# Kernel tuning notes

Measured on AMD Instinct MI355X. Metric: run time of the kernel, lower is better.

The kernel has to match this reference:

```python
import jax, jax.numpy as jnp
import numpy as np

HEAD_DIM = 64
EMBED_DIM = 1024

def setup_inputs() -> dict:
    key = jax.random.key(0)
    k1, k2, k3, k4 = jax.random.split(key, 4)
    x = jax.random.normal(k1, (4, 4096, EMBED_DIM), dtype=jnp.float32)
    # nn.Linear(embed_dim, head_dim, bias=False): weight shape (head_dim, embed_dim)
    s = 1.0 / np.sqrt(EMBED_DIM)
    Wq = jax.random.uniform(k2, (HEAD_DIM, EMBED_DIM), jnp.float32, -s, s)
    Wk = jax.random.uniform(k3, (HEAD_DIM, EMBED_DIM), jnp.float32, -s, s)
    Wv = jax.random.uniform(k4, (HEAD_DIM, EMBED_DIM), jnp.float32, -s, s)
    return {"x": x, "Wq": Wq, "Wk": Wk, "Wv": Wv}

def reference(x, Wq, Wk, Wv):
    # Faithful to source: V = self.key(x), i.e. uses Wk (Wv is an unused param).
    n_ctx = x.shape[1]
    Q = jnp.einsum('bse,de->bsd', x, Wq)
    K = jnp.einsum('bse,de->bsd', x, Wk)
    V = jnp.einsum('bse,de->bsd', x, Wk)
    scale = 1.0 / jnp.sqrt(jnp.asarray(K.shape[-1], x.dtype))
    scores = jnp.einsum('bqd,bkd->bqk', Q, K) * scale  # [b, n_ctx, n_ctx]
    causal = jnp.tril(jnp.ones((n_ctx, n_ctx), dtype=bool))
    scores = jnp.where(causal, scores, jnp.asarray(-jnp.inf, scores.dtype))
    attn = jax.nn.softmax(scores, axis=-1)
    # dropout(p=0.2) omitted: reference runs in eval mode (identity)
    out = jnp.einsum('bqk,bkd->bqd', attn, V)
    return out
```

## Files before the change

kernel.cpp:

```cpp
#include <hip/hip_runtime.h>

typedef _Float16 f16;
typedef _Float16 f16x8 __attribute__((ext_vector_type(8)));
typedef _Float16 f16x4 __attribute__((ext_vector_type(4)));
typedef float f32x4 __attribute__((ext_vector_type(4)));

#define S_LEN 4096
#define B_SZ  4
#define E_DIM 1024
#define D_DIM 64
#define NROWS (B_SZ * S_LEN)
#define QSCALE (0.125f * 1.44269504088896f)
#define SMAX 8.0f

__device__ __forceinline__ float exp2g(float x) { return __builtin_amdgcn_exp2f(x); }

__global__ __launch_bounds__(256) void wpack_kernel(const float* __restrict__ Wq,
                                                    const float* __restrict__ Wk,
                                                    f16* __restrict__ Bp) {
    int id = blockIdx.x * 256 + threadIdx.x;
    int lane = id & 63, kc = (id >> 6) & 31, n = id >> 11;
    int row = n * 16 + (lane & 15);
    int col = kc * 32 + (lane >> 4) * 8;
    const float* src = (row < 64) ? (Wq + (long)row * E_DIM + col)
                                  : (Wk + (long)(row - 64) * E_DIM + col);
    float4 v0 = ((const float4*)src)[0];
    float4 v1 = ((const float4*)src)[1];
    f16x8 h = {(f16)v0.x, (f16)v0.y, (f16)v0.z, (f16)v0.w,
               (f16)v1.x, (f16)v1.y, (f16)v1.z, (f16)v1.w};
    *(f16x8*)(Bp + (long)id * 8) = h;
}

__global__ __launch_bounds__(512, 2) void proj_kernel(const float* __restrict__ x,
                                                      const f16* __restrict__ Bp,
                                                      f16* __restrict__ Qh,
                                                      f16* __restrict__ Khp,
                                                      f16* __restrict__ Kvp) {
    __shared__ union {
        float xs[2][64][68];
        float ro[8][16][68];
    } sm;

    const int tid  = threadIdx.x;
    const int wav  = tid >> 6;
    const int w_m  = wav >> 1;
    const int w_n  = wav & 1;
    const int lane = tid & 63;
    const int l15  = lane & 15;
    const int quad = lane >> 4;
    const long m0  = (long)blockIdx.x * 64;

    f32x4 acc[4];
#pragma unroll
    for (int n = 0; n < 4; n++) acc[n] = (f32x4){0.f, 0.f, 0.f, 0.f};

    float4 ra[2];
    const int r0[2]  = { (tid * 2 + 0) >> 4,  (tid * 2 + 1) >> 4 };
    (void)r0;

#pragma unroll
    for (int j = 0; j < 2; j++) {
        int idx = j * 512 + tid;
        int row = idx >> 4, c4 = idx & 15;
        ra[j] = *(const float4*)(x + (m0 + row) * E_DIM + c4 * 4);
    }
#pragma unroll
    for (int j = 0; j < 2; j++) {
        int idx = j * 512 + tid;
        int row = idx >> 4, c4 = idx & 15;
        *(f32x4*)&sm.xs[0][row][c4 * 4] = (f32x4){ra[j].x, ra[j].y, ra[j].z, ra[j].w};
    }
    __syncthreads();

    for (int c = 0; c < 16; c++) {
        const int cur = c & 1;
        if (c + 1 < 16) {
#pragma unroll
            for (int j = 0; j < 2; j++) {
                int idx = j * 512 + tid;
                int row = idx >> 4, c4 = idx & 15;
                ra[j] = *(const float4*)(x + (m0 + row) * E_DIM + (c + 1) * 64 + c4 * 4);
            }
        }
#pragma unroll
        for (int kf = 0; kf < 2; kf++) {
            f32x4 a0 = *(const f32x4*)&sm.xs[cur][w_m * 16 + l15][kf * 32 + quad * 8];
            f32x4 a1 = *(const f32x4*)&sm.xs[cur][w_m * 16 + l15][kf * 32 + quad * 8 + 4];
            f16x8 A = {(f16)a0[0], (f16)a0[1], (f16)a0[2], (f16)a0[3],
                       (f16)a1[0], (f16)a1[1], (f16)a1[2], (f16)a1[3]};
            const int kc = c * 2 + kf;
#pragma unroll
            for (int nn = 0; nn < 4; nn++) {
                const int n = w_n * 4 + nn;
                f16x8 B = *(const f16x8*)(Bp + (((long)n * 32 + kc) * 64 + lane) * 8);
                acc[nn] = __builtin_amdgcn_mfma_f32_16x16x32_f16(A, B, acc[nn], 0, 0, 0);
            }
        }
        if (c + 1 < 16) {
#pragma unroll
            for (int j = 0; j < 2; j++) {
                int idx = j * 512 + tid;
                int row = idx >> 4, c4 = idx & 15;
                *(f32x4*)&sm.xs[cur ^ 1][row][c4 * 4] = (f32x4){ra[j].x, ra[j].y, ra[j].z, ra[j].w};
            }
        }
        __syncthreads();
    }

    const int s = wav;
#pragma unroll
    for (int nn = 0; nn < 4; nn++)
#pragma unroll
        for (int r = 0; r < 4; r++)
            sm.ro[s][quad * 4 + r][nn * 16 + l15] = acc[nn][r];
    __syncthreads();

    if (w_n == 0) {
        float q[16];
#pragma unroll
        for (int g = 0; g < 4; g++)
            *(f32x4*)&q[g * 4] = *(const f32x4*)&sm.ro[s][l15][quad * 16 + g * 4];
        f16 o[16];
#pragma unroll
        for (int i = 0; i < 16; i++) o[i] = (f16)(q[i] * QSCALE);
        f16* dst = Qh + (m0 + w_m * 16 + l15) * 64 + quad * 16;
        *(f16x8*)dst       = *(f16x8*)&o[0];
        *(f16x8*)(dst + 8) = *(f16x8*)&o[8];
    } else {
        const long chunk = blockIdx.x;
#pragma unroll
        for (int kf = 0; kf < 2; kf++) {
            f32x4 k0 = *(const f32x4*)&sm.ro[s][l15][kf * 32 + quad * 8];
            f32x4 k1 = *(const f32x4*)&sm.ro[s][l15][kf * 32 + quad * 8 + 4];
            f16x8 h = {(f16)k0[0], (f16)k0[1], (f16)k0[2], (f16)k0[3],
                       (f16)k1[0], (f16)k1[1], (f16)k1[2], (f16)k1[3]};
            *(f16x8*)(Khp + chunk * 4096 + (w_m * 2 + kf) * 512 + lane * 8) = h;
        }
        f16 t16[16];
#pragma unroll
        for (int nn = 0; nn < 4; nn++)
#pragma unroll
            for (int j = 0; j < 4; j++)
                t16[nn * 4 + j] = (f16)sm.ro[s][quad * 4 + j][nn * 16 + l15];
        f16* dst = Kvp + chunk * 4096 + w_m * 1024 + lane * 16;
        *(f16x8*)dst       = *(f16x8*)&t16[0];
        *(f16x8*)(dst + 8) = *(f16x8*)&t16[8];
    }
}

__global__ __launch_bounds__(256, 2) void attn_kernel(const f16* __restrict__ Qh,
                                                      const f16* __restrict__ Khp,
                                                      const f16* __restrict__ Kvp,
                                                      float* __restrict__ Out) {
    __shared__ float Ro[4][32][68];
    __shared__ float Rl[4][32];

    const int tid  = threadIdx.x;
    const int w    = tid >> 6;
    const int lane = tid & 63;
    const int l15  = lane & 15;
    const int quad = lane >> 4;

    const int bid = blockIdx.x;
    int q32, b;
    if (bid < 256) { q32 = 127 - (bid >> 2); b = bid & 3; }
    else           { int k = bid - 256; q32 = k >> 2; b = k & 3; }
    const int q0   = q32 * 32;
    const int jmax = q32 >> 1;

    const f16* Qb = Qh + (long)b * S_LEN * 64;
    f16x8 Aq[2][2];
#pragma unroll
    for (int g = 0; g < 2; g++)
#pragma unroll
        for (int kf = 0; kf < 2; kf++)
            Aq[g][kf] = *(const f16x8*)(Qb + (long)(q0 + g * 16 + l15) * 64 + kf * 32 + quad * 8);

    const f16x4 ones = {(f16)1.f, (f16)1.f, (f16)1.f, (f16)1.f};
    f32x4 O[2][4];
    f32x4 Lacc[2];
#pragma unroll
    for (int g = 0; g < 2; g++) {
        Lacc[g] = (f32x4){0.f, 0.f, 0.f, 0.f};
#pragma unroll
        for (int n = 0; n < 4; n++) O[g][n] = (f32x4){0.f, 0.f, 0.f, 0.f};
    }

    const long cb = (long)b * 64;

#define LOADKA(buf, jj)                                                        \
    {                                                                          \
        const f16* p_ = Khp + (cb + (jj)) * 4096 + lane * 8;                   \
        _Pragma("unroll")                                                      \
        for (int q8 = 0; q8 < 8; q8++) buf[q8] = *(const f16x8*)(p_ + q8 * 512);\
    }

#define COMPUTE(buf, jj)                                                       \
    {                                                                          \
        const f16* kv_ = Kvp + (cb + (jj)) * 4096 + lane * 16;                 \
        const int tlim = ((jj) == jmax) ? (((q0 + 31 - jmax * 64) >> 4) + 1) : 4; \
        _Pragma("unroll")                                                      \
        for (int t = 0; t < 4; t++) {                                          \
            if (t < tlim) {                                                    \
                f32x4 St0 = (f32x4){0.f, 0.f, 0.f, 0.f};                       \
                f32x4 St1 = (f32x4){0.f, 0.f, 0.f, 0.f};                       \
                St0 = __builtin_amdgcn_mfma_f32_16x16x32_f16(buf[t * 2],     Aq[0][0], St0, 0, 0, 0); \
                St0 = __builtin_amdgcn_mfma_f32_16x16x32_f16(buf[t * 2 + 1], Aq[0][1], St0, 0, 0, 0); \
                St1 = __builtin_amdgcn_mfma_f32_16x16x32_f16(buf[t * 2],     Aq[1][0], St1, 0, 0, 0); \
                St1 = __builtin_amdgcn_mfma_f32_16x16x32_f16(buf[t * 2 + 1], Aq[1][1], St1, 0, 0, 0); \
                if ((jj) == jmax) {                                            \
                    int kc_ = jmax * 64 + t * 16 + quad * 4;                   \
                    _Pragma("unroll")                                          \
                    for (int r = 0; r < 4; r++) {                              \
                        if (kc_ + r > q0 + l15)      St0[r] = -1e30f;          \
                        if (kc_ + r > q0 + 16 + l15) St1[r] = -1e30f;          \
                    }                                                          \
                }                                                              \
                f16x4 P0, P1;                                                  \
                _Pragma("unroll")                                              \
                for (int r = 0; r < 4; r++) {                                  \
                    P0[r] = (f16)exp2g(St0[r] - SMAX);                         \
                    P1[r] = (f16)exp2g(St1[r] - SMAX);                         \
                }                                                              \
                Lacc[0] = __builtin_amdgcn_mfma_f32_16x16x16f16(P0, ones, Lacc[0], 0, 0, 0); \
                Lacc[1] = __builtin_amdgcn_mfma_f32_16x16x16f16(P1, ones, Lacc[1], 0, 0, 0); \
                f16x8 v0 = *(const f16x8*)(kv_ + t * 1024);                    \
                f16x8 v1 = *(const f16x8*)(kv_ + t * 1024 + 8);                \
                f16x4 b0 = __builtin_shufflevector(v0, v0, 0, 1, 2, 3);        \
                f16x4 b1 = __builtin_shufflevector(v0, v0, 4, 5, 6, 7);        \
                f16x4 b2 = __builtin_shufflevector(v1, v1, 0, 1, 2, 3);        \
                f16x4 b3 = __builtin_shufflevector(v1, v1, 4, 5, 6, 7);        \
                O[0][0] = __builtin_amdgcn_mfma_f32_16x16x16f16(P0, b0, O[0][0], 0, 0, 0); \
                O[0][1] = __builtin_amdgcn_mfma_f32_16x16x16f16(P0, b1, O[0][1], 0, 0, 0); \
                O[0][2] = __builtin_amdgcn_mfma_f32_16x16x16f16(P0, b2, O[0][2], 0, 0, 0); \
                O[0][3] = __builtin_amdgcn_mfma_f32_16x16x16f16(P0, b3, O[0][3], 0, 0, 0); \
                O[1][0] = __builtin_amdgcn_mfma_f32_16x16x16f16(P1, b0, O[1][0], 0, 0, 0); \
                O[1][1] = __builtin_amdgcn_mfma_f32_16x16x16f16(P1, b1, O[1][1], 0, 0, 0); \
                O[1][2] = __builtin_amdgcn_mfma_f32_16x16x16f16(P1, b2, O[1][2], 0, 0, 0); \
                O[1][3] = __builtin_amdgcn_mfma_f32_16x16x16f16(P1, b3, O[1][3], 0, 0, 0); \
            }                                                                  \
        }                                                                      \
    }

    f16x8 kaA[8], kaB[8];
    int j = w;
    if (j <= jmax) LOADKA(kaA, j);
    while (j <= jmax) {
        if (j + 4 <= jmax) LOADKA(kaB, j + 4);
        COMPUTE(kaA, j);
        j += 4;
        if (j > jmax) break;
        if (j + 4 <= jmax) LOADKA(kaA, j + 4);
        COMPUTE(kaB, j);
        j += 4;
    }
#undef LOADKA
#undef COMPUTE

#pragma unroll
    for (int g = 0; g < 2; g++) {
#pragma unroll
        for (int n = 0; n < 4; n++)
#pragma unroll
            for (int r = 0; r < 4; r++)
                Ro[w][g * 16 + quad * 4 + r][n * 16 + l15] = O[g][n][r];
        if (l15 == 0)
#pragma unroll
            for (int r = 0; r < 4; r++)
                Rl[w][g * 16 + quad * 4 + r] = Lacc[g][r];
    }
    __syncthreads();

    const int row = tid >> 3;
    const int c0  = (tid & 7) * 8;
    float sum[8];
#pragma unroll
    for (int i = 0; i < 8; i++) sum[i] = 0.f;
    float lt = 0.f;
#pragma unroll
    for (int w4 = 0; w4 < 4; w4++) {
        lt += Rl[w4][row];
#pragma unroll
        for (int g4 = 0; g4 < 2; g4++) {
            f32x4 u = *(const f32x4*)&Ro[w4][row][c0 + g4 * 4];
#pragma unroll
            for (int i = 0; i < 4; i++) sum[g4 * 4 + i] += u[i];
        }
    }
    float inv = 1.0f / lt;
    float* dst = Out + ((long)b * S_LEN + q0 + row) * 64 + c0;
    *(float4*)dst       = make_float4(sum[0] * inv, sum[1] * inv, sum[2] * inv, sum[3] * inv);
    *(float4*)(dst + 4) = make_float4(sum[4] * inv, sum[5] * inv, sum[6] * inv, sum[7] * inv);
}

extern "C" void kernel_launch(void* const* d_in, const int* in_sizes, int n_in,
                              void* d_out, int out_size, void* d_ws, size_t ws_size,
                              hipStream_t stream) {
    const float* x  = (const float*)d_in[0];
    const float* Wq = (const float*)d_in[1];
    const float* Wk = (const float*)d_in[2];
    float* out = (float*)d_out;

    f16* Qh  = (f16*)d_ws;
    f16* Bp  = Qh + (long)NROWS * D_DIM;
    f16* Khp = Bp + (long)128 * E_DIM;
    f16* Kvp = Khp + (long)NROWS * D_DIM;

    wpack_kernel<<<dim3(64), dim3(256), 0, stream>>>(Wq, Wk, Bp);
    proj_kernel<<<dim3(NROWS / 64), dim3(512), 0, stream>>>(x, Bp, Qh, Khp, Kvp);
    attn_kernel<<<dim3(B_SZ * 128), dim3(256), 0, stream>>>(Qh, Khp, Kvp, out);
}
```

Baseline: 155.6 us.

## Prefetch V tiles with K in attention; halve projection block size

```diff
diff --git a/kernel.cpp b/kernel.cpp
--- a/kernel.cpp
+++ b/kernel.cpp
@@ -31,42 +31,39 @@
     *(f16x8*)(Bp + (long)id * 8) = h;
 }
 
-__global__ __launch_bounds__(512, 2) void proj_kernel(const float* __restrict__ x,
-                                                      const f16* __restrict__ Bp,
-                                                      f16* __restrict__ Qh,
-                                                      f16* __restrict__ Khp,
-                                                      f16* __restrict__ Kvp) {
+__global__ __launch_bounds__(256) void proj_kernel(const float* __restrict__ x,
+                                                   const f16* __restrict__ Bp,
+                                                   f16* __restrict__ Qh,
+                                                   f16* __restrict__ Khp,
+                                                   f16* __restrict__ Kvp) {
     __shared__ union {
-        float xs[2][64][68];
-        float ro[8][16][68];
+        float xs[2][32][68];
+        float ro[4][16][68];
     } sm;
 
     const int tid  = threadIdx.x;
-    const int wav  = tid >> 6;
-    const int w_m  = wav >> 1;
-    const int w_n  = wav & 1;
+    const int w    = tid >> 6;
+    const int w_m  = w >> 1;
+    const int w_n  = w & 1;
     const int lane = tid & 63;
     const int l15  = lane & 15;
     const int quad = lane >> 4;
-    const long m0  = (long)blockIdx.x * 64;
+    const long m0  = (long)blockIdx.x * 32;
 
     f32x4 acc[4];
 #pragma unroll
     for (int n = 0; n < 4; n++) acc[n] = (f32x4){0.f, 0.f, 0.f, 0.f};
 
     float4 ra[2];
-    const int r0[2]  = { (tid * 2 + 0) >> 4,  (tid * 2 + 1) >> 4 };
-    (void)r0;
-
 #pragma unroll
     for (int j = 0; j < 2; j++) {
-        int idx = j * 512 + tid;
+        int idx = j * 256 + tid;
         int row = idx >> 4, c4 = idx & 15;
         ra[j] = *(const float4*)(x + (m0 + row) * E_DIM + c4 * 4);
     }
 #pragma unroll
     for (int j = 0; j < 2; j++) {
-        int idx = j * 512 + tid;
+        int idx = j * 256 + tid;
         int row = idx >> 4, c4 = idx & 15;
         *(f32x4*)&sm.xs[0][row][c4 * 4] = (f32x4){ra[j].x, ra[j].y, ra[j].z, ra[j].w};
     }
@@ -77,7 +74,7 @@
         if (c + 1 < 16) {
 #pragma unroll
             for (int j = 0; j < 2; j++) {
-                int idx = j * 512 + tid;
+                int idx = j * 256 + tid;
                 int row = idx >> 4, c4 = idx & 15;
                 ra[j] = *(const float4*)(x + (m0 + row) * E_DIM + (c + 1) * 64 + c4 * 4);
             }
@@ -99,7 +96,7 @@
         if (c + 1 < 16) {
 #pragma unroll
             for (int j = 0; j < 2; j++) {
-                int idx = j * 512 + tid;
+                int idx = j * 256 + tid;
                 int row = idx >> 4, c4 = idx & 15;
                 *(f32x4*)&sm.xs[cur ^ 1][row][c4 * 4] = (f32x4){ra[j].x, ra[j].y, ra[j].z, ra[j].w};
             }
@@ -107,19 +104,18 @@
         __syncthreads();
     }
 
-    const int s = wav;
 #pragma unroll
     for (int nn = 0; nn < 4; nn++)
 #pragma unroll
         for (int r = 0; r < 4; r++)
-            sm.ro[s][quad * 4 + r][nn * 16 + l15] = acc[nn][r];
+            sm.ro[w][quad * 4 + r][nn * 16 + l15] = acc[nn][r];
     __syncthreads();
 
     if (w_n == 0) {
         float q[16];
 #pragma unroll
         for (int g = 0; g < 4; g++)
-            *(f32x4*)&q[g * 4] = *(const f32x4*)&sm.ro[s][l15][quad * 16 + g * 4];
+            *(f32x4*)&q[g * 4] = *(const f32x4*)&sm.ro[w][l15][quad * 16 + g * 4];
         f16 o[16];
 #pragma unroll
         for (int i = 0; i < 16; i++) o[i] = (f16)(q[i] * QSCALE);
@@ -127,31 +123,32 @@
         *(f16x8*)dst       = *(f16x8*)&o[0];
         *(f16x8*)(dst + 8) = *(f16x8*)&o[8];
     } else {
-        const long chunk = blockIdx.x;
+        const long chunk = blockIdx.x >> 1;
+        const int  t     = (blockIdx.x & 1) * 2 + w_m;
 #pragma unroll
         for (int kf = 0; kf < 2; kf++) {
-            f32x4 k0 = *(const f32x4*)&sm.ro[s][l15][kf * 32 + quad * 8];
-            f32x4 k1 = *(const f32x4*)&sm.ro[s][l15][kf * 32 + quad * 8 + 4];
+            f32x4 k0 = *(const f32x4*)&sm.ro[w][l15][kf * 32 + quad * 8];
+            f32x4 k1 = *(const f32x4*)&sm.ro[w][l15][kf * 32 + quad * 8 + 4];
             f16x8 h = {(f16)k0[0], (f16)k0[1], (f16)k0[2], (f16)k0[3],
                        (f16)k1[0], (f16)k1[1], (f16)k1[2], (f16)k1[3]};
-            *(f16x8*)(Khp + chunk * 4096 + (w_m * 2 + kf) * 512 + lane * 8) = h;
+            *(f16x8*)(Khp + chunk * 4096 + (t * 2 + kf) * 512 + lane * 8) = h;
         }
         f16 t16[16];
 #pragma unroll
         for (int nn = 0; nn < 4; nn++)
 #pragma unroll
             for (int j = 0; j < 4; j++)
-                t16[nn * 4 + j] = (f16)sm.ro[s][quad * 4 + j][nn * 16 + l15];
-        f16* dst = Kvp + chunk * 4096 + w_m * 1024 + lane * 16;
+                t16[nn * 4 + j] = (f16)sm.ro[w][quad * 4 + j][nn * 16 + l15];
+        f16* dst = Kvp + chunk * 4096 + t * 1024 + lane * 16;
         *(f16x8*)dst       = *(f16x8*)&t16[0];
         *(f16x8*)(dst + 8) = *(f16x8*)&t16[8];
     }
 }
 
-__global__ __launch_bounds__(256, 2) void attn_kernel(const f16* __restrict__ Qh,
-                                                      const f16* __restrict__ Khp,
-                                                      const f16* __restrict__ Kvp,
-                                                      float* __restrict__ Out) {
+__global__ __launch_bounds__(256) void attn_kernel(const f16* __restrict__ Qh,
+                                                   const f16* __restrict__ Khp,
+                                                   const f16* __restrict__ Kvp,
+                                                   float* __restrict__ Out) {
     __shared__ float Ro[4][32][68];
     __shared__ float Rl[4][32];
 
@@ -188,26 +185,31 @@
 
     const long cb = (long)b * 64;
 
-#define LOADKA(buf, jj)                                                        \
+#define LOADK(bufa, bufv, jj)                                                  \
     {                                                                          \
-        const f16* p_ = Khp + (cb + (jj)) * 4096 + lane * 8;                   \
+        const f16* pa_ = Khp + (cb + (jj)) * 4096 + lane * 8;                  \
         _Pragma("unroll")                                                      \
-        for (int q8 = 0; q8 < 8; q8++) buf[q8] = *(const f16x8*)(p_ + q8 * 512);\
-    }
-
-#define COMPUTE(buf, jj)                                                       \
+        for (int q8 = 0; q8 < 8; q8++) bufa[q8] = *(const f16x8*)(pa_ + q8 * 512); \
+        const f16* pv_ = Kvp + (cb + (jj)) * 4096 + lane * 16;                 \
+        _Pragma("unroll")                                                      \
+        for (int t = 0; t < 4; t++) {                                          \
+            bufv[t * 2]     = *(const f16x8*)(pv_ + t * 1024);                 \
+            bufv[t * 2 + 1] = *(const f16x8*)(pv_ + t * 1024 + 8);             \
+        }                                                                      \
+    }
+
+#define COMPUTE(bufa, bufv, jj)                                                \
     {                                                                          \
-        const f16* kv_ = Kvp + (cb + (jj)) * 4096 + lane * 16;                 \
         const int tlim = ((jj) == jmax) ? (((q0 + 31 - jmax * 64) >> 4) + 1) : 4; \
         _Pragma("unroll")                                                      \
         for (int t = 0; t < 4; t++) {                                          \
             if (t < tlim) {                                                    \
                 f32x4 St0 = (f32x4){0.f, 0.f, 0.f, 0.f};                       \
                 f32x4 St1 = (f32x4){0.f, 0.f, 0.f, 0.f};                       \
-                St0 = __builtin_amdgcn_mfma_f32_16x16x32_f16(buf[t * 2],     Aq[0][0], St0, 0, 0, 0); \
-                St0 = __builtin_amdgcn_mfma_f32_16x16x32_f16(buf[t * 2 + 1], Aq[0][1], St0, 0, 0, 0); \
-                St1 = __builtin_amdgcn_mfma_f32_16x16x32_f16(buf[t * 2],     Aq[1][0], St1, 0, 0, 0); \
-                St1 = __builtin_amdgcn_mfma_f32_16x16x32_f16(buf[t * 2 + 1], Aq[1][1], St1, 0, 0, 0); \
+                St0 = __builtin_amdgcn_mfma_f32_16x16x32_f16(bufa[t * 2],     Aq[0][0], St0, 0, 0, 0); \
+                St0 = __builtin_amdgcn_mfma_f32_16x16x32_f16(bufa[t * 2 + 1], Aq[0][1], St0, 0, 0, 0); \
+                St1 = __builtin_amdgcn_mfma_f32_16x16x32_f16(bufa[t * 2],     Aq[1][0], St1, 0, 0, 0); \
+                St1 = __builtin_amdgcn_mfma_f32_16x16x32_f16(bufa[t * 2 + 1], Aq[1][1], St1, 0, 0, 0); \
                 if ((jj) == jmax) {                                            \
                     int kc_ = jmax * 64 + t * 16 + quad * 4;                   \
                     _Pragma("unroll")                                          \
@@ -224,12 +226,10 @@
                 }                                                              \
                 Lacc[0] = __builtin_amdgcn_mfma_f32_16x16x16f16(P0, ones, Lacc[0], 0, 0, 0); \
                 Lacc[1] = __builtin_amdgcn_mfma_f32_16x16x16f16(P1, ones, Lacc[1], 0, 0, 0); \
-                f16x8 v0 = *(const f16x8*)(kv_ + t * 1024);                    \
-                f16x8 v1 = *(const f16x8*)(kv_ + t * 1024 + 8);                \
-                f16x4 b0 = __builtin_shufflevector(v0, v0, 0, 1, 2, 3);        \
-                f16x4 b1 = __builtin_shufflevector(v0, v0, 4, 5, 6, 7);        \
-                f16x4 b2 = __builtin_shufflevector(v1, v1, 0, 1, 2, 3);        \
-                f16x4 b3 = __builtin_shufflevector(v1, v1, 4, 5, 6, 7);        \
+                f16x4 b0 = __builtin_shufflevector(bufv[t * 2],     bufv[t * 2],     0, 1, 2, 3); \
+                f16x4 b1 = __builtin_shufflevector(bufv[t * 2],     bufv[t * 2],     4, 5, 6, 7); \
+                f16x4 b2 = __builtin_shufflevector(bufv[t * 2 + 1], bufv[t * 2 + 1], 0, 1, 2, 3); \
+                f16x4 b3 = __builtin_shufflevector(bufv[t * 2 + 1], bufv[t * 2 + 1], 4, 5, 6, 7); \
                 O[0][0] = __builtin_amdgcn_mfma_f32_16x16x16f16(P0, b0, O[0][0], 0, 0, 0); \
                 O[0][1] = __builtin_amdgcn_mfma_f32_16x16x16f16(P0, b1, O[0][1], 0, 0, 0); \
                 O[0][2] = __builtin_amdgcn_mfma_f32_16x16x16f16(P0, b2, O[0][2], 0, 0, 0); \
@@ -242,19 +242,19 @@
         }                                                                      \
     }
 
-    f16x8 kaA[8], kaB[8];
+    f16x8 kaA[8], kaB[8], kvA[8], kvB[8];
     int j = w;
-    if (j <= jmax) LOADKA(kaA, j);
+    if (j <= jmax) LOADK(kaA, kvA, j);
     while (j <= jmax) {
-        if (j + 4 <= jmax) LOADKA(kaB, j + 4);
-        COMPUTE(kaA, j);
+        if (j + 4 <= jmax) LOADK(kaB, kvB, j + 4);
+        COMPUTE(kaA, kvA, j);
         j += 4;
         if (j > jmax) break;
-        if (j + 4 <= jmax) LOADKA(kaA, j + 4);
-        COMPUTE(kaB, j);
+        if (j + 4 <= jmax) LOADK(kaA, kvA, j + 4);
+        COMPUTE(kaB, kvB, j);
         j += 4;
     }
-#undef LOADKA
+#undef LOADK
 #undef COMPUTE
 
 #pragma unroll
@@ -307,6 +307,6 @@
     f16* Kvp = Khp + (long)NROWS * D_DIM;
 
     wpack_kernel<<<dim3(64), dim3(256), 0, stream>>>(Wq, Wk, Bp);
-    proj_kernel<<<dim3(NROWS / 64), dim3(512), 0, stream>>>(x, Bp, Qh, Khp, Kvp);
+    proj_kernel<<<dim3(NROWS / 32), dim3(256), 0, stream>>>(x, Bp, Qh, Khp, Kvp);
     attn_kernel<<<dim3(B_SZ * 128), dim3(256), 0, stream>>>(Qh, Khp, Kvp, out);
 }
```

After: 138.6 us. 1.12x faster.
